# Performance work log

Hardware: AMD Instinct MI355X
Metric: run time of the kernel (lower is better)

The kernel has to match this reference:

```python
import jax, jax.numpy as jnp
import numpy as np

N_B, N_A = 32, 48
H_IN, E_IN, H_H, H_G, NCELLS = 64, 32, 64, 16, 5


def setup_inputs() -> dict:
    key = jax.random.key(0)
    ks = jax.random.split(key, 10)
    A = (jax.random.uniform(ks[0], (N_B, N_A, N_A)) < 0.3).astype(jnp.float32)
    h = jax.random.normal(ks[1], (N_B, N_A, H_IN), dtype=jnp.float32)
    E = jax.random.normal(ks[2], (N_B, N_A, N_A, E_IN), dtype=jnp.float32)
    s_h = 1.0 / np.sqrt(H_IN)
    s_e = 1.0 / np.sqrt(E_IN)
    s_g = 1.0 / np.sqrt(H_H)
    W_h = jax.random.uniform(ks[3], (H_IN, H_H), minval=-s_h, maxval=s_h)
    b_h = jax.random.uniform(ks[4], (H_H,), minval=-s_h, maxval=s_h)
    W_e = jax.random.uniform(ks[5], (E_IN, H_G * H_H), minval=-s_e, maxval=s_e)
    b_e = jax.random.uniform(ks[6], (H_G * H_H,), minval=-s_e, maxval=s_e)
    W_ih = jax.random.uniform(ks[7], (3 * H_H, H_G), minval=-s_g, maxval=s_g)
    W_hh = jax.random.uniform(ks[8], (3 * H_H, H_H), minval=-s_g, maxval=s_g)
    b_ih = jax.random.uniform(jax.random.fold_in(key, 11), (3 * H_H,), minval=-s_g, maxval=s_g)
    b_hh = jax.random.uniform(jax.random.fold_in(key, 12), (3 * H_H,), minval=-s_g, maxval=s_g)
    return {"A": A, "h": h, "E": E, "W_h": W_h, "b_h": b_h, "W_e": W_e, "b_e": b_e,
            "W_ih": W_ih, "b_ih": b_ih, "W_hh": W_hh, "b_hh": b_hh}


def _gru_cell(x, hprev, W_ih, b_ih, W_hh, b_hh):
    # PyTorch GRUCell semantics
    gi = x @ W_ih.T + b_ih      # [N, 3*H_H]
    gh = hprev @ W_hh.T + b_hh  # [N, 3*H_H]
    i_r, i_z, i_n = jnp.split(gi, 3, axis=-1)
    h_r, h_z, h_n = jnp.split(gh, 3, axis=-1)
    r = jax.nn.sigmoid(i_r + h_r)
    z = jax.nn.sigmoid(i_z + h_z)
    n = jnp.tanh(i_n + r * h_n)
    return (1.0 - z) * n + z * hprev


def reference(A, h, E, W_h, b_h, W_e, b_e, W_ih, b_ih, W_hh, b_hh):
    N_b, n_a = h.shape[0], A.shape[1]
    maskh = (jnp.sum(A, axis=-1, keepdims=True) > 0.1).astype(jnp.float32)  # [B,n,1]
    hv = jax.nn.relu(h @ W_h + b_h) * maskh                                 # [B,n,H_H]
    Ee = jax.nn.relu(E @ W_e + b_e).reshape(N_b, n_a, n_a, H_G, H_H)
    Ee = Ee * A[..., None, None]                                            # mask edges
    # E.matmul(h).sum(dim=1) == (sum_i E[b,i,j]) @ h[b,j]; precompute the i-sum
    Esum = Ee.sum(axis=1)                                                   # [B,j,G,H]
    hc = hv  # [B,n,H_H]
    for _ in range(NCELLS):
        M = jnp.einsum('bjgh,bjh->bjg', Esum, hc).reshape(N_b * n_a, H_G)
        hc = _gru_cell(M, hc.reshape(N_b * n_a, H_H), W_ih, b_ih, W_hh, b_hh)
        hc = hc.reshape(N_b, n_a, H_H)
    return hc
```

## Files before the change

### kernel.cpp

```cpp
#include <hip/hip_runtime.h>
#include <stdint.h>

#define NB 32
#define NA 48
#define HIN 64
#define EIN 32
#define HH 64
#define HG 16
#define NCELLS 5
#define GH 1024
#define EROW 40
#define P3 3
#define ESTR 1088

typedef __attribute__((ext_vector_type(8))) short short8;
typedef __attribute__((ext_vector_type(4))) float float4v;

__device__ __forceinline__ unsigned short f2bf(float f) {
    union { float f; unsigned int u; } v; v.f = f;
    unsigned int u = v.u + 0x7FFF + ((v.u >> 16) & 1);
    return (unsigned short)(u >> 16);
}
__device__ __forceinline__ float bf2f(unsigned short s) {
    union { unsigned int u; float f; } v; v.u = ((unsigned int)s) << 16;
    return v.f;
}

__global__ __launch_bounds__(256) void swizzle_We(const float* __restrict__ W_e,
                                                  unsigned short* __restrict__ hiB,
                                                  unsigned short* __restrict__ loB) {
    const int o  = blockIdx.x * 256 + threadIdx.x;
    const int ct = o >> 9;
    const int l  = (o >> 3) & 63;
    const int jj = o & 7;
    const int k  = (l >> 4) * 8 + jj;
    const int c  = ct * 16 + (l & 15);
    const float x = W_e[k * GH + c];
    const unsigned short hb = f2bf(x);
    hiB[o] = hb;
    loB[o] = f2bf(x - bf2f(hb));
}

__global__ __launch_bounds__(256) void prep_gw(const float* __restrict__ W_ih,
                                               const float* __restrict__ W_hh,
                                               float4* __restrict__ gw4) {
    const int idx = blockIdx.x * 256 + threadIdx.x;
    if (idx >= 20 * 192) return;
    const int j = idx / 192;
    const int c = idx - j * 192;
    float4 v;
    if (j < 4)  v = *(const float4*)(W_ih + c * HG + 4 * j);
    else        v = *(const float4*)(W_hh + c * HH + 4 * (j - 4));
    gw4[idx] = v;
}

template <int NTMAX>
__device__ __forceinline__ void edge_phase3(
    const unsigned short* __restrict__ hiB, const unsigned short* __restrict__ loB,
    const float* __restrict__ b_e,
    const unsigned short* EcolH, const unsigned short* EcolL,
    const float* mask_s,
    int wave, int lane, int mrow, int quad,
    float* Esum_s)
{
    const float4v zero4 = {0.0f, 0.0f, 0.0f, 0.0f};
    short8 aH[P3][NTMAX ? NTMAX : 1], aL[P3][NTMAX ? NTMAX : 1];
    #pragma unroll
    for (int p = 0; p < P3; ++p)
        #pragma unroll
        for (int rt = 0; rt < NTMAX; ++rt) {
            const int off = (p * 48 + 16 * rt + mrow) * EROW + quad * 8;
            aH[p][rt] = *(const short8*)(EcolH + off);
            aL[p][rt] = *(const short8*)(EcolL + off);
        }

    #pragma unroll 2
    for (int t = 0; t < 16; ++t) {
        const int ct = wave * 16 + t;
        const short8 bfH = *(const short8*)(hiB + (size_t)ct * 512 + lane * 8);
        const short8 bfL = *(const short8*)(loB + (size_t)ct * 512 + lane * 8);
        const float be = b_e[ct * 16 + mrow];
        float psum[P3] = {0.0f, 0.0f, 0.0f};
        #pragma unroll
        for (int p = 0; p < P3; ++p) {
            #pragma unroll
            for (int rt = 0; rt < NTMAX; ++rt) {
                float4v d = __builtin_amdgcn_mfma_f32_16x16x32_bf16(aL[p][rt], bfH, zero4, 0, 0, 0);
                d = __builtin_amdgcn_mfma_f32_16x16x32_bf16(aH[p][rt], bfL, d, 0, 0, 0);
                d = __builtin_amdgcn_mfma_f32_16x16x32_bf16(aH[p][rt], bfH, d, 0, 0, 0);
                const float4v mk = *(const float4v*)(mask_s + p * 48 + rt * 16 + quad * 4);
                #pragma unroll
                for (int rg = 0; rg < 4; ++rg)
                    psum[p] = fmaf(fmaxf(d[rg] + be, 0.0f), mk[rg], psum[p]);
            }
        }
        #pragma unroll
        for (int p = 0; p < P3; ++p) {
            float ps = psum[p];
            ps += __shfl_xor(ps, 16);
            ps += __shfl_xor(ps, 32);
            if (lane < 16) {
                const int c = ct * 16 + lane;
                Esum_s[p * ESTR + (c >> 6) * 68 + (c & 63)] = ps;
            }
        }
    }
}

__global__ __launch_bounds__(256, 2) void fused_kernel(
    const float* __restrict__ A,  const float* __restrict__ h,
    const float* __restrict__ E,
    const float* __restrict__ W_h, const float* __restrict__ b_h,
    const float* __restrict__ b_e,
    const float* __restrict__ b_ih, const float* __restrict__ b_hh,
    const unsigned short* __restrict__ hiB, const unsigned short* __restrict__ loB,
    const float4* __restrict__ gw4,
    float* __restrict__ out)
{
    __shared__ unsigned short EcolH[P3 * NA * EROW];
    __shared__ unsigned short EcolL[P3 * NA * EROW];
    __shared__ float Esum_s[P3 * ESTR];
    __shared__ float mask_s[P3 * 48];
    __shared__ int   ilist[P3 * NA];
    __shared__ int   cnt_s[P3];
    __shared__ float hc_s[P3 * HH];
    __shared__ float M_s[P3 * HG];
    __shared__ float gsum_s[P3 * 2 * HH];
    __shared__ float gin_s[P3 * HH], ghn_s[P3 * HH];

    const int node0 = blockIdx.x * P3;
    const int b = node0 / NA, j0 = node0 - b * NA;
    const int tid = threadIdx.x, lane = tid & 63, wave = tid >> 6;
    const int mrow = lane & 15, quad = lane >> 4;

    if (wave < P3) {
        const float a = (lane < NA) ? A[((size_t)b * NA + lane) * NA + (j0 + wave)] : 0.0f;
        const unsigned long long m = __ballot(a != 0.0f);
        if (a != 0.0f) ilist[wave * NA + __popcll(m & ((1ull << lane) - 1ull))] = lane;
        if (lane == 0) cnt_s[wave] = (int)__popcll(m);
    }
    __syncthreads();

    for (int idx = tid; idx < P3 * NA * 8; idx += 256) {
        const int p = idx / (NA * 8);
        const int rem = idx - p * (NA * 8);
        const int r = rem >> 3, q = rem & 7;
        uint2 hv2 = make_uint2(0u, 0u), lv2 = make_uint2(0u, 0u);
        if (r < cnt_s[p]) {
            const int i = ilist[p * NA + r];
            const float4 ev = *(const float4*)(E + ((size_t)(b * NA + i) * NA + (j0 + p)) * EIN + 4 * q);
            unsigned short h0 = f2bf(ev.x), h1 = f2bf(ev.y), h2 = f2bf(ev.z), h3 = f2bf(ev.w);
            unsigned short l0 = f2bf(ev.x - bf2f(h0)), l1 = f2bf(ev.y - bf2f(h1));
            unsigned short l2 = f2bf(ev.z - bf2f(h2)), l3 = f2bf(ev.w - bf2f(h3));
            hv2 = make_uint2((unsigned int)h0 | ((unsigned int)h1 << 16),
                             (unsigned int)h2 | ((unsigned int)h3 << 16));
            lv2 = make_uint2((unsigned int)l0 | ((unsigned int)l1 << 16),
                             (unsigned int)l2 | ((unsigned int)l3 << 16));
        }
        *(uint2*)(&EcolH[(p * NA + r) * EROW + 4 * q]) = hv2;
        *(uint2*)(&EcolL[(p * NA + r) * EROW + 4 * q]) = lv2;
    }
    if (tid < P3 * 48) {
        const int p = tid / 48, rem = tid - p * 48;
        mask_s[tid] = (rem < cnt_s[p]) ? 1.0f : 0.0f;
    }
    __syncthreads();

    const int nt0 = (cnt_s[0] + 15) >> 4, nt1 = (cnt_s[1] + 15) >> 4, nt2 = (cnt_s[2] + 15) >> 4;
    int ntmax = nt0 > nt1 ? nt0 : nt1; ntmax = ntmax > nt2 ? ntmax : nt2;

    if (ntmax == 0)
        edge_phase3<0>(hiB, loB, b_e, EcolH, EcolL, mask_s, wave, lane, mrow, quad, Esum_s);
    else if (ntmax == 1)
        edge_phase3<1>(hiB, loB, b_e, EcolH, EcolL, mask_s, wave, lane, mrow, quad, Esum_s);
    else if (ntmax == 2)
        edge_phase3<2>(hiB, loB, b_e, EcolH, EcolL, mask_s, wave, lane, mrow, quad, Esum_s);
    else
        edge_phase3<3>(hiB, loB, b_e, EcolH, EcolL, mask_s, wave, lane, mrow, quad, Esum_s);

    float bihc = 0.0f, bhhc = 0.0f;
    if (tid < 3 * HH) { bihc = b_ih[tid]; bhhc = b_hh[tid]; }

    if (wave < P3) {
        const int node = node0 + wave;
        const float a = (lane < NA) ? A[(size_t)node * NA + lane] : 0.0f;
        const unsigned long long mrowm = __ballot(a != 0.0f);
        const float maskh = (mrowm != 0ull) ? 1.0f : 0.0f;
        const float hr = h[(size_t)node * HIN + lane];
        float acc = b_h[lane];
        #pragma unroll
        for (int k = 0; k < HIN; ++k)
            acc = fmaf(__shfl(hr, k), W_h[k * HH + lane], acc);
        hc_s[wave * HH + lane] = fmaxf(acc, 0.0f) * maskh;
    }
    __syncthreads();

    #pragma unroll 1
    for (int it = 0; it < NCELLS; ++it) {
        if (tid < 192) {
            const int p = tid >> 6, s = tid & 63, g = s >> 2, q = s & 3;
            const float* ep = Esum_s + p * ESTR + g * 68 + q * 16;
            const float* hp = hc_s + p * HH + q * 16;
            const float4v e0 = *(const float4v*)(ep),     h0 = *(const float4v*)(hp);
            const float4v e1 = *(const float4v*)(ep + 4), h1 = *(const float4v*)(hp + 4);
            const float4v e2 = *(const float4v*)(ep + 8), h2 = *(const float4v*)(hp + 8);
            const float4v e3 = *(const float4v*)(ep + 12), h3 = *(const float4v*)(hp + 12);
            float pp = e0[0] * h0[0];
            pp = fmaf(e0[1], h0[1], pp); pp = fmaf(e0[2], h0[2], pp); pp = fmaf(e0[3], h0[3], pp);
            pp = fmaf(e1[0], h1[0], pp); pp = fmaf(e1[1], h1[1], pp);
            pp = fmaf(e1[2], h1[2], pp); pp = fmaf(e1[3], h1[3], pp);
            pp = fmaf(e2[0], h2[0], pp); pp = fmaf(e2[1], h2[1], pp);
            pp = fmaf(e2[2], h2[2], pp); pp = fmaf(e2[3], h2[3], pp);
            pp = fmaf(e3[0], h3[0], pp); pp = fmaf(e3[1], h3[1], pp);
            pp = fmaf(e3[2], h3[2], pp); pp = fmaf(e3[3], h3[3], pp);
            pp += __shfl_xor(pp, 1);
            pp += __shfl_xor(pp, 2);
            if (q == 0) M_s[p * HG + g] = pp;
        }
        __syncthreads();
        if (tid < 192) {
            const float4* gp = gw4 + tid;
            float gi0 = bihc, gi1 = bihc, gi2 = bihc;
            #pragma unroll
            for (int jj = 0; jj < 4; ++jj) {
                const float4 w = gp[jj * 192];
                const float4v m0 = *(const float4v*)(M_s + 0 * HG + 4 * jj);
                const float4v m1 = *(const float4v*)(M_s + 1 * HG + 4 * jj);
                const float4v m2 = *(const float4v*)(M_s + 2 * HG + 4 * jj);
                gi0 = fmaf(m0[0], w.x, gi0); gi0 = fmaf(m0[1], w.y, gi0);
                gi0 = fmaf(m0[2], w.z, gi0); gi0 = fmaf(m0[3], w.w, gi0);
                gi1 = fmaf(m1[0], w.x, gi1); gi1 = fmaf(m1[1], w.y, gi1);
                gi1 = fmaf(m1[2], w.z, gi1); gi1 = fmaf(m1[3], w.w, gi1);
                gi2 = fmaf(m2[0], w.x, gi2); gi2 = fmaf(m2[1], w.y, gi2);
                gi2 = fmaf(m2[2], w.z, gi2); gi2 = fmaf(m2[3], w.w, gi2);
            }
            float gh0 = bhhc, gh1 = bhhc, gh2 = bhhc;
            #pragma unroll
            for (int jj = 4; jj < 20; ++jj) {
                const float4 w = gp[jj * 192];
                const float4v h0 = *(const float4v*)(hc_s + 0 * HH + 4 * (jj - 4));
                const float4v h1 = *(const float4v*)(hc_s + 1 * HH + 4 * (jj - 4));
                const float4v h2 = *(const float4v*)(hc_s + 2 * HH + 4 * (jj - 4));
                gh0 = fmaf(h0[0], w.x, gh0); gh0 = fmaf(h0[1], w.y, gh0);
                gh0 = fmaf(h0[2], w.z, gh0); gh0 = fmaf(h0[3], w.w, gh0);
                gh1 = fmaf(h1[0], w.x, gh1); gh1 = fmaf(h1[1], w.y, gh1);
                gh1 = fmaf(h1[2], w.z, gh1); gh1 = fmaf(h1[3], w.w, gh1);
                gh2 = fmaf(h2[0], w.x, gh2); gh2 = fmaf(h2[1], w.y, gh2);
                gh2 = fmaf(h2[2], w.z, gh2); gh2 = fmaf(h2[3], w.w, gh2);
            }
            if (tid < 2 * HH) {
                gsum_s[0 * 2 * HH + tid] = gi0 + gh0;
                gsum_s[1 * 2 * HH + tid] = gi1 + gh1;
                gsum_s[2 * 2 * HH + tid] = gi2 + gh2;
            } else {
                const int c = tid - 2 * HH;
                gin_s[0 * HH + c] = gi0; ghn_s[0 * HH + c] = gh0;
                gin_s[1 * HH + c] = gi1; ghn_s[1 * HH + c] = gh1;
                gin_s[2 * HH + c] = gi2; ghn_s[2 * HH + c] = gh2;
            }
        }
        __syncthreads();
        if (tid < 192) {
            const int p = tid >> 6, c = tid & 63;
            const float r = 1.0f / (1.0f + __expf(-gsum_s[p * 2 * HH + c]));
            const float z = 1.0f / (1.0f + __expf(-gsum_s[p * 2 * HH + HH + c]));
            const float nin = gin_s[p * HH + c] + r * ghn_s[p * HH + c];
            const float n = 1.0f - 2.0f / (__expf(2.0f * nin) + 1.0f);
            hc_s[p * HH + c] = (1.0f - z) * n + z * hc_s[p * HH + c];
        }
        __syncthreads();
    }

    if (tid < 192) out[(size_t)node0 * HH + tid] = hc_s[tid];
}

extern "C" void kernel_launch(void* const* d_in, const int* in_sizes, int n_in,
                              void* d_out, int out_size, void* d_ws, size_t ws_size,
                              hipStream_t stream) {
    const float* A    = (const float*)d_in[0];
    const float* h    = (const float*)d_in[1];
    const float* E    = (const float*)d_in[2];
    const float* W_h  = (const float*)d_in[3];
    const float* b_h  = (const float*)d_in[4];
    const float* W_e  = (const float*)d_in[5];
    const float* b_e  = (const float*)d_in[6];
    const float* W_ih = (const float*)d_in[7];
    const float* b_ih = (const float*)d_in[8];
    const float* W_hh = (const float*)d_in[9];
    const float* b_hh = (const float*)d_in[10];
    unsigned short* hiB = (unsigned short*)d_ws;
    unsigned short* loB = hiB + 32768;
    float4* gw4 = (float4*)(loB + 32768);
    float* out = (float*)d_out;

    hipLaunchKernelGGL(swizzle_We, dim3(128), dim3(256), 0, stream, W_e, hiB, loB);
    hipLaunchKernelGGL(prep_gw, dim3(15), dim3(256), 0, stream, W_ih, W_hh, gw4);
    hipLaunchKernelGGL(fused_kernel, dim3(NB * NA / P3), dim3(256), 0, stream,
                       A, h, E, W_h, b_h, b_e, b_ih, b_hh, hiB, loB, gw4, out);
}
```

Before: 113.4 us.

## Process six nodes per block with one wave per node and wave-local GRU

Merges the two prep kernels into one launch and doubles nodes per block to six, using 384 threads so each wave owns one node. The edge phase drops the per-row mask and instead subtracts the padded rows' relu(bias) contribution analytically. Each wave keeps its Esum slice in registers and runs the GRU cell iterations independently, with no block-wide barriers in the loop. GRU weights are staged in shared memory. The larger shared-memory footprint (about 60KB for gw_sf) may reduce occupancy.

```diff
diff --git a/kernel.cpp b/kernel.cpp
--- a/kernel.cpp
+++ b/kernel.cpp
@@ -10,8 +10,8 @@
 #define NCELLS 5
 #define GH 1024
 #define EROW 40
-#define P3 3
-#define ESTR 1088
+#define P6 6
+#define EMW 20
 
 typedef __attribute__((ext_vector_type(8))) short short8;
 typedef __attribute__((ext_vector_type(4))) float float4v;
@@ -26,88 +26,84 @@
     return v.f;
 }
 
-__global__ __launch_bounds__(256) void swizzle_We(const float* __restrict__ W_e,
-                                                  unsigned short* __restrict__ hiB,
-                                                  unsigned short* __restrict__ loB) {
-    const int o  = blockIdx.x * 256 + threadIdx.x;
-    const int ct = o >> 9;
-    const int l  = (o >> 3) & 63;
-    const int jj = o & 7;
-    const int k  = (l >> 4) * 8 + jj;
-    const int c  = ct * 16 + (l & 15);
-    const float x = W_e[k * GH + c];
-    const unsigned short hb = f2bf(x);
-    hiB[o] = hb;
-    loB[o] = f2bf(x - bf2f(hb));
-}
-
-__global__ __launch_bounds__(256) void prep_gw(const float* __restrict__ W_ih,
-                                               const float* __restrict__ W_hh,
-                                               float4* __restrict__ gw4) {
+__global__ __launch_bounds__(256) void prep(const float* __restrict__ W_e,
+                                            const float* __restrict__ W_ih,
+                                            const float* __restrict__ W_hh,
+                                            unsigned short* __restrict__ hiB,
+                                            unsigned short* __restrict__ loB,
+                                            float4* __restrict__ gw4) {
     const int idx = blockIdx.x * 256 + threadIdx.x;
-    if (idx >= 20 * 192) return;
-    const int j = idx / 192;
-    const int c = idx - j * 192;
-    float4 v;
-    if (j < 4)  v = *(const float4*)(W_ih + c * HG + 4 * j);
-    else        v = *(const float4*)(W_hh + c * HH + 4 * (j - 4));
-    gw4[idx] = v;
-}
-
-template <int NTMAX>
-__device__ __forceinline__ void edge_phase3(
+    if (idx < 32768) {
+        const int ct = idx >> 9, l = (idx >> 3) & 63, jj = idx & 7;
+        const int k = (l >> 4) * 8 + jj;
+        const int c = ct * 16 + (l & 15);
+        const float x = W_e[k * GH + c];
+        const unsigned short hb = f2bf(x);
+        hiB[idx] = hb;
+        loB[idx] = f2bf(x - bf2f(hb));
+    } else {
+        const int o = idx - 32768;
+        if (o < 20 * 192) {
+            const int j = o / 192, c = o - j * 192;
+            float4 v;
+            if (j < 4)  v = *(const float4*)(W_ih + c * HG + 4 * j);
+            else        v = *(const float4*)(W_hh + c * HH + 4 * (j - 4));
+            gw4[o] = v;
+        }
+    }
+}
+
+template <int NT>
+__device__ __forceinline__ void edge6(
     const unsigned short* __restrict__ hiB, const unsigned short* __restrict__ loB,
     const float* __restrict__ b_e,
     const unsigned short* EcolH, const unsigned short* EcolL,
-    const float* mask_s,
-    int wave, int lane, int mrow, int quad,
-    float* Esum_s)
+    const int* cnt_s, float* em_s,
+    int wave, int lane, int mrow, int quad)
 {
     const float4v zero4 = {0.0f, 0.0f, 0.0f, 0.0f};
-    short8 aH[P3][NTMAX ? NTMAX : 1], aL[P3][NTMAX ? NTMAX : 1];
+    short8 aH[P6][NT ? NT : 1], aL[P6][NT ? NT : 1];
+    float finv[P6];
     #pragma unroll
-    for (int p = 0; p < P3; ++p)
-        #pragma unroll
-        for (int rt = 0; rt < NTMAX; ++rt) {
-            const int off = (p * 48 + 16 * rt + mrow) * EROW + quad * 8;
+    for (int p = 0; p < P6; ++p) {
+        finv[p] = (float)(16 * NT - cnt_s[p]);
+        #pragma unroll
+        for (int rt = 0; rt < NT; ++rt) {
+            const int off = (p * NA + 16 * rt + mrow) * EROW + quad * 8;
             aH[p][rt] = *(const short8*)(EcolH + off);
             aL[p][rt] = *(const short8*)(EcolL + off);
         }
-
-    #pragma unroll 2
-    for (int t = 0; t < 16; ++t) {
-        const int ct = wave * 16 + t;
+    }
+    #pragma unroll 1
+    for (int ct = wave; ct < 64; ct += P6) {
         const short8 bfH = *(const short8*)(hiB + (size_t)ct * 512 + lane * 8);
         const short8 bfL = *(const short8*)(loB + (size_t)ct * 512 + lane * 8);
         const float be = b_e[ct * 16 + mrow];
-        float psum[P3] = {0.0f, 0.0f, 0.0f};
-        #pragma unroll
-        for (int p = 0; p < P3; ++p) {
+        const float bneg = fmaxf(be, 0.0f);
+        const int ldst = (16 * (ct & 3) + (ct >> 2)) * EMW;
+        #pragma unroll
+        for (int p = 0; p < P6; ++p) {
+            float ps = 0.0f;
             #pragma unroll
-            for (int rt = 0; rt < NTMAX; ++rt) {
+            for (int rt = 0; rt < NT; ++rt) {
                 float4v d = __builtin_amdgcn_mfma_f32_16x16x32_bf16(aL[p][rt], bfH, zero4, 0, 0, 0);
                 d = __builtin_amdgcn_mfma_f32_16x16x32_bf16(aH[p][rt], bfL, d, 0, 0, 0);
                 d = __builtin_amdgcn_mfma_f32_16x16x32_bf16(aH[p][rt], bfH, d, 0, 0, 0);
-                const float4v mk = *(const float4v*)(mask_s + p * 48 + rt * 16 + quad * 4);
-                #pragma unroll
-                for (int rg = 0; rg < 4; ++rg)
-                    psum[p] = fmaf(fmaxf(d[rg] + be, 0.0f), mk[rg], psum[p]);
+                ps += fmaxf(d[0] + be, 0.0f);
+                ps += fmaxf(d[1] + be, 0.0f);
+                ps += fmaxf(d[2] + be, 0.0f);
+                ps += fmaxf(d[3] + be, 0.0f);
             }
-        }
-        #pragma unroll
-        for (int p = 0; p < P3; ++p) {
-            float ps = psum[p];
             ps += __shfl_xor(ps, 16);
             ps += __shfl_xor(ps, 32);
-            if (lane < 16) {
-                const int c = ct * 16 + lane;
-                Esum_s[p * ESTR + (c >> 6) * 68 + (c & 63)] = ps;
-            }
-        }
-    }
-}
-
-__global__ __launch_bounds__(256, 2) void fused_kernel(
+            ps = fmaf(finv[p], -bneg, ps);
+            if (lane < 16)
+                em_s[p * 1280 + ldst + lane] = ps;
+        }
+    }
+}
+
+__global__ __launch_bounds__(384, 2) void fused_kernel(
     const float* __restrict__ A,  const float* __restrict__ h,
     const float* __restrict__ E,
     const float* __restrict__ W_h, const float* __restrict__ b_h,
@@ -117,23 +113,21 @@
     const float4* __restrict__ gw4,
     float* __restrict__ out)
 {
-    __shared__ unsigned short EcolH[P3 * NA * EROW];
-    __shared__ unsigned short EcolL[P3 * NA * EROW];
-    __shared__ float Esum_s[P3 * ESTR];
-    __shared__ float mask_s[P3 * 48];
-    __shared__ int   ilist[P3 * NA];
-    __shared__ int   cnt_s[P3];
-    __shared__ float hc_s[P3 * HH];
-    __shared__ float M_s[P3 * HG];
-    __shared__ float gsum_s[P3 * 2 * HH];
-    __shared__ float gin_s[P3 * HH], ghn_s[P3 * HH];
-
-    const int node0 = blockIdx.x * P3;
+    __shared__ float gw_sf[20 * 192 * 4];
+    __shared__ unsigned short EcolH[P6 * NA * EROW];
+    __shared__ unsigned short EcolL[P6 * NA * EROW];
+    __shared__ float em_s[P6 * 1280];
+    __shared__ float hcbuf[P6 * HH];
+    __shared__ float Mbuf[P6 * HG];
+    __shared__ int   ilist[P6 * NA];
+    __shared__ int   cnt_s[P6];
+
+    const int node0 = blockIdx.x * P6;
     const int b = node0 / NA, j0 = node0 - b * NA;
     const int tid = threadIdx.x, lane = tid & 63, wave = tid >> 6;
     const int mrow = lane & 15, quad = lane >> 4;
 
-    if (wave < P3) {
+    {
         const float a = (lane < NA) ? A[((size_t)b * NA + lane) * NA + (j0 + wave)] : 0.0f;
         const unsigned long long m = __ballot(a != 0.0f);
         if (a != 0.0f) ilist[wave * NA + __popcll(m & ((1ull << lane) - 1ull))] = lane;
@@ -141,7 +135,9 @@
     }
     __syncthreads();
 
-    for (int idx = tid; idx < P3 * NA * 8; idx += 256) {
+    for (int idx = tid; idx < 20 * 192; idx += 384)
+        *(float4*)(gw_sf + idx * 4) = gw4[idx];
+    for (int idx = tid; idx < P6 * NA * 8; idx += 384) {
         const int p = idx / (NA * 8);
         const int rem = idx - p * (NA * 8);
         const int r = rem >> 3, q = rem & 7;
@@ -160,29 +156,29 @@
         *(uint2*)(&EcolH[(p * NA + r) * EROW + 4 * q]) = hv2;
         *(uint2*)(&EcolL[(p * NA + r) * EROW + 4 * q]) = lv2;
     }
-    if (tid < P3 * 48) {
-        const int p = tid / 48, rem = tid - p * 48;
-        mask_s[tid] = (rem < cnt_s[p]) ? 1.0f : 0.0f;
-    }
     __syncthreads();
 
-    const int nt0 = (cnt_s[0] + 15) >> 4, nt1 = (cnt_s[1] + 15) >> 4, nt2 = (cnt_s[2] + 15) >> 4;
-    int ntmax = nt0 > nt1 ? nt0 : nt1; ntmax = ntmax > nt2 ? ntmax : nt2;
-
+    int ntmax = 0;
+    #pragma unroll
+    for (int p = 0; p < P6; ++p) {
+        const int nt = (cnt_s[p] + 15) >> 4;
+        ntmax = nt > ntmax ? nt : ntmax;
+    }
     if (ntmax == 0)
-        edge_phase3<0>(hiB, loB, b_e, EcolH, EcolL, mask_s, wave, lane, mrow, quad, Esum_s);
+        edge6<0>(hiB, loB, b_e, EcolH, EcolL, cnt_s, em_s, wave, lane, mrow, quad);
     else if (ntmax == 1)
-        edge_phase3<1>(hiB, loB, b_e, EcolH, EcolL, mask_s, wave, lane, mrow, quad, Esum_s);
+        edge6<1>(hiB, loB, b_e, EcolH, EcolL, cnt_s, em_s, wave, lane, mrow, quad);
     else if (ntmax == 2)
-        edge_phase3<2>(hiB, loB, b_e, EcolH, EcolL, mask_s, wave, lane, mrow, quad, Esum_s);
+        edge6<2>(hiB, loB, b_e, EcolH, EcolL, cnt_s, em_s, wave, lane, mrow, quad);
     else
-        edge_phase3<3>(hiB, loB, b_e, EcolH, EcolL, mask_s, wave, lane, mrow, quad, Esum_s);
-
-    float bihc = 0.0f, bhhc = 0.0f;
-    if (tid < 3 * HH) { bihc = b_ih[tid]; bhhc = b_hh[tid]; }
-
-    if (wave < P3) {
-        const int node = node0 + wave;
+        edge6<3>(hiB, loB, b_e, EcolH, EcolL, cnt_s, em_s, wave, lane, mrow, quad);
+
+    if (ntmax == 0)
+        for (int idx = tid; idx < P6 * 1280; idx += 384) em_s[idx] = 0.0f;
+
+    const int node = node0 + wave;
+    float hc;
+    {
         const float a = (lane < NA) ? A[(size_t)node * NA + lane] : 0.0f;
         const unsigned long long mrowm = __ballot(a != 0.0f);
         const float maskh = (mrowm != 0ull) ? 1.0f : 0.0f;
@@ -191,87 +187,80 @@
         #pragma unroll
         for (int k = 0; k < HIN; ++k)
             acc = fmaf(__shfl(hr, k), W_h[k * HH + lane], acc);
-        hc_s[wave * HH + lane] = fmaxf(acc, 0.0f) * maskh;
+        hc = fmaxf(acc, 0.0f) * maskh;
     }
     __syncthreads();
+
+    float4v em4[4];
+    #pragma unroll
+    for (int kk = 0; kk < 4; ++kk)
+        em4[kk] = *(const float4v*)(em_s + wave * 1280 + lane * EMW + 4 * kk);
+    const float bihr = b_ih[lane], bihz = b_ih[HH + lane], bihn = b_ih[2 * HH + lane];
+    const float bhhr = b_hh[lane], bhhz = b_hh[HH + lane], bhhn = b_hh[2 * HH + lane];
+    float* hcb = hcbuf + wave * HH;
+    float* Mb  = Mbuf + wave * HG;
+    const int q16 = quad * 16;
 
     #pragma unroll 1
     for (int it = 0; it < NCELLS; ++it) {
-        if (tid < 192) {
-            const int p = tid >> 6, s = tid & 63, g = s >> 2, q = s & 3;
-            const float* ep = Esum_s + p * ESTR + g * 68 + q * 16;
-            const float* hp = hc_s + p * HH + q * 16;
-            const float4v e0 = *(const float4v*)(ep),     h0 = *(const float4v*)(hp);
-            const float4v e1 = *(const float4v*)(ep + 4), h1 = *(const float4v*)(hp + 4);
-            const float4v e2 = *(const float4v*)(ep + 8), h2 = *(const float4v*)(hp + 8);
-            const float4v e3 = *(const float4v*)(ep + 12), h3 = *(const float4v*)(hp + 12);
-            float pp = e0[0] * h0[0];
-            pp = fmaf(e0[1], h0[1], pp); pp = fmaf(e0[2], h0[2], pp); pp = fmaf(e0[3], h0[3], pp);
-            pp = fmaf(e1[0], h1[0], pp); pp = fmaf(e1[1], h1[1], pp);
-            pp = fmaf(e1[2], h1[2], pp); pp = fmaf(e1[3], h1[3], pp);
-            pp = fmaf(e2[0], h2[0], pp); pp = fmaf(e2[1], h2[1], pp);
-            pp = fmaf(e2[2], h2[2], pp); pp = fmaf(e2[3], h2[3], pp);
-            pp = fmaf(e3[0], h3[0], pp); pp = fmaf(e3[1], h3[1], pp);
-            pp = fmaf(e3[2], h3[2], pp); pp = fmaf(e3[3], h3[3], pp);
-            pp += __shfl_xor(pp, 1);
-            pp += __shfl_xor(pp, 2);
-            if (q == 0) M_s[p * HG + g] = pp;
-        }
-        __syncthreads();
-        if (tid < 192) {
-            const float4* gp = gw4 + tid;
-            float gi0 = bihc, gi1 = bihc, gi2 = bihc;
-            #pragma unroll
-            for (int jj = 0; jj < 4; ++jj) {
-                const float4 w = gp[jj * 192];
-                const float4v m0 = *(const float4v*)(M_s + 0 * HG + 4 * jj);
-                const float4v m1 = *(const float4v*)(M_s + 1 * HG + 4 * jj);
-                const float4v m2 = *(const float4v*)(M_s + 2 * HG + 4 * jj);
-                gi0 = fmaf(m0[0], w.x, gi0); gi0 = fmaf(m0[1], w.y, gi0);
-                gi0 = fmaf(m0[2], w.z, gi0); gi0 = fmaf(m0[3], w.w, gi0);
-                gi1 = fmaf(m1[0], w.x, gi1); gi1 = fmaf(m1[1], w.y, gi1);
-                gi1 = fmaf(m1[2], w.z, gi1); gi1 = fmaf(m1[3], w.w, gi1);
-                gi2 = fmaf(m2[0], w.x, gi2); gi2 = fmaf(m2[1], w.y, gi2);
-                gi2 = fmaf(m2[2], w.z, gi2); gi2 = fmaf(m2[3], w.w, gi2);
-            }
-            float gh0 = bhhc, gh1 = bhhc, gh2 = bhhc;
-            #pragma unroll
-            for (int jj = 4; jj < 20; ++jj) {
-                const float4 w = gp[jj * 192];
-                const float4v h0 = *(const float4v*)(hc_s + 0 * HH + 4 * (jj - 4));
-                const float4v h1 = *(const float4v*)(hc_s + 1 * HH + 4 * (jj - 4));
-                const float4v h2 = *(const float4v*)(hc_s + 2 * HH + 4 * (jj - 4));
-                gh0 = fmaf(h0[0], w.x, gh0); gh0 = fmaf(h0[1], w.y, gh0);
-                gh0 = fmaf(h0[2], w.z, gh0); gh0 = fmaf(h0[3], w.w, gh0);
-                gh1 = fmaf(h1[0], w.x, gh1); gh1 = fmaf(h1[1], w.y, gh1);
-                gh1 = fmaf(h1[2], w.z, gh1); gh1 = fmaf(h1[3], w.w, gh1);
-                gh2 = fmaf(h2[0], w.x, gh2); gh2 = fmaf(h2[1], w.y, gh2);
-                gh2 = fmaf(h2[2], w.z, gh2); gh2 = fmaf(h2[3], w.w, gh2);
-            }
-            if (tid < 2 * HH) {
-                gsum_s[0 * 2 * HH + tid] = gi0 + gh0;
-                gsum_s[1 * 2 * HH + tid] = gi1 + gh1;
-                gsum_s[2 * 2 * HH + tid] = gi2 + gh2;
-            } else {
-                const int c = tid - 2 * HH;
-                gin_s[0 * HH + c] = gi0; ghn_s[0 * HH + c] = gh0;
-                gin_s[1 * HH + c] = gi1; ghn_s[1 * HH + c] = gh1;
-                gin_s[2 * HH + c] = gi2; ghn_s[2 * HH + c] = gh2;
-            }
-        }
-        __syncthreads();
-        if (tid < 192) {
-            const int p = tid >> 6, c = tid & 63;
-            const float r = 1.0f / (1.0f + __expf(-gsum_s[p * 2 * HH + c]));
-            const float z = 1.0f / (1.0f + __expf(-gsum_s[p * 2 * HH + HH + c]));
-            const float nin = gin_s[p * HH + c] + r * ghn_s[p * HH + c];
-            const float n = 1.0f - 2.0f / (__expf(2.0f * nin) + 1.0f);
-            hc_s[p * HH + c] = (1.0f - z) * n + z * hc_s[p * HH + c];
-        }
-        __syncthreads();
-    }
-
-    if (tid < 192) out[(size_t)node0 * HH + tid] = hc_s[tid];
+        hcb[lane] = hc;
+        float pp;
+        {
+            const float4v ha = *(const float4v*)(hcb + q16);
+            const float4v hb = *(const float4v*)(hcb + q16 + 4);
+            const float4v hcv = *(const float4v*)(hcb + q16 + 8);
+            const float4v hd = *(const float4v*)(hcb + q16 + 12);
+            pp = em4[0][0] * ha[0];
+            pp = fmaf(em4[0][1], ha[1], pp); pp = fmaf(em4[0][2], ha[2], pp); pp = fmaf(em4[0][3], ha[3], pp);
+            pp = fmaf(em4[1][0], hb[0], pp); pp = fmaf(em4[1][1], hb[1], pp);
+            pp = fmaf(em4[1][2], hb[2], pp); pp = fmaf(em4[1][3], hb[3], pp);
+            pp = fmaf(em4[2][0], hcv[0], pp); pp = fmaf(em4[2][1], hcv[1], pp);
+            pp = fmaf(em4[2][2], hcv[2], pp); pp = fmaf(em4[2][3], hcv[3], pp);
+            pp = fmaf(em4[3][0], hd[0], pp); pp = fmaf(em4[3][1], hd[1], pp);
+            pp = fmaf(em4[3][2], hd[2], pp); pp = fmaf(em4[3][3], hd[3], pp);
+        }
+        pp += __shfl_xor(pp, 16);
+        pp += __shfl_xor(pp, 32);
+        if (lane < 16) Mb[lane] = pp;
+        float4v M4[4];
+        #pragma unroll
+        for (int kk = 0; kk < 4; ++kk) M4[kk] = *(const float4v*)(Mb + 4 * kk);
+
+        float gir = bihr, giz = bihz, gin = bihn;
+        #pragma unroll
+        for (int j = 0; j < 4; ++j) {
+            const float4v wr = *(const float4v*)(gw_sf + (j * 192 + lane) * 4);
+            const float4v wz = *(const float4v*)(gw_sf + (j * 192 + 64 + lane) * 4);
+            const float4v wn = *(const float4v*)(gw_sf + (j * 192 + 128 + lane) * 4);
+            gir = fmaf(M4[j][0], wr[0], gir); gir = fmaf(M4[j][1], wr[1], gir);
+            gir = fmaf(M4[j][2], wr[2], gir); gir = fmaf(M4[j][3], wr[3], gir);
+            giz = fmaf(M4[j][0], wz[0], giz); giz = fmaf(M4[j][1], wz[1], giz);
+            giz = fmaf(M4[j][2], wz[2], giz); giz = fmaf(M4[j][3], wz[3], giz);
+            gin = fmaf(M4[j][0], wn[0], gin); gin = fmaf(M4[j][1], wn[1], gin);
+            gin = fmaf(M4[j][2], wn[2], gin); gin = fmaf(M4[j][3], wn[3], gin);
+        }
+        float ghr = bhhr, ghz = bhhz, ghn = bhhn;
+        #pragma unroll
+        for (int j = 0; j < 16; ++j) {
+            const float4v h4 = *(const float4v*)(hcb + 4 * j);
+            const float4v wr = *(const float4v*)(gw_sf + ((j + 4) * 192 + lane) * 4);
+            const float4v wz = *(const float4v*)(gw_sf + ((j + 4) * 192 + 64 + lane) * 4);
+            const float4v wn = *(const float4v*)(gw_sf + ((j + 4) * 192 + 128 + lane) * 4);
+            ghr = fmaf(h4[0], wr[0], ghr); ghr = fmaf(h4[1], wr[1], ghr);
+            ghr = fmaf(h4[2], wr[2], ghr); ghr = fmaf(h4[3], wr[3], ghr);
+            ghz = fmaf(h4[0], wz[0], ghz); ghz = fmaf(h4[1], wz[1], ghz);
+            ghz = fmaf(h4[2], wz[2], ghz); ghz = fmaf(h4[3], wz[3], ghz);
+            ghn = fmaf(h4[0], wn[0], ghn); ghn = fmaf(h4[1], wn[1], ghn);
+            ghn = fmaf(h4[2], wn[2], ghn); ghn = fmaf(h4[3], wn[3], ghn);
+        }
+        const float r = 1.0f / (1.0f + __expf(-(gir + ghr)));
+        const float z = 1.0f / (1.0f + __expf(-(giz + ghz)));
+        const float nin = gin + r * ghn;
+        const float n = 1.0f - 2.0f / (__expf(2.0f * nin) + 1.0f);
+        hc = (1.0f - z) * n + z * hc;
+    }
+
+    out[(size_t)node * HH + lane] = hc;
 }
 
 extern "C" void kernel_launch(void* const* d_in, const int* in_sizes, int n_in,
@@ -293,8 +282,8 @@
     float4* gw4 = (float4*)(loB + 32768);
     float* out = (float*)d_out;
 
-    hipLaunchKernelGGL(swizzle_We, dim3(128), dim3(256), 0, stream, W_e, hiB, loB);
-    hipLaunchKernelGGL(prep_gw, dim3(15), dim3(256), 0, stream, W_ih, W_hh, gw4);
-    hipLaunchKernelGGL(fused_kernel, dim3(NB * NA / P3), dim3(256), 0, stream,
+    hipLaunchKernelGGL(prep, dim3(144), dim3(256), 0, stream,
+                       W_e, W_ih, W_hh, hiB, loB, gw4);
+    hipLaunchKernelGGL(fused_kernel, dim3(NB * NA / P6), dim3(384), 0, stream,
                        A, h, E, W_h, b_h, b_e, b_ih, b_hh, hiB, loB, gw4, out);
 }
```

After: 127.1 us. 1.12x slower.
